# Kernel optimization log

Hardware: AMD Instinct MI355X
Metric: run time of the kernel (lower is better)

The kernel has to match this reference:

```python
import jax, jax.numpy as jnp
import numpy as np

B, CF, CC, H, W = 4, 64, 128, 512, 512
NUM_POINTS = 4096
OVERSAMPLE = 3
BETA = 0.75
HIDDEN = 256
OUT_CH = 4
IN_FEATS = CF + CC


def grid_sample_points(img, coords):
    """Bilinear sample img [B,C,H,W] at coords [B,N,2] in [0,1] (x,y order),
    matching F.grid_sample(align_corners=False, padding_mode='zeros') after
    the 2*coords-1 normalization in point_sample."""
    Bb, C, Hh, Ww = img.shape
    # unnormalize: ((2c-1)+1)*size/2 - 0.5 == c*size - 0.5
    x = coords[..., 0] * Ww - 0.5
    y = coords[..., 1] * Hh - 0.5
    x0 = jnp.floor(x)
    y0 = jnp.floor(y)
    wx1 = x - x0  # [B,N]
    wy1 = y - y0
    x0i = x0.astype(jnp.int32)
    y0i = y0.astype(jnp.int32)
    flat = img.reshape(Bb, C, Hh * Ww)

    def gather(xi, yi):
        valid = (xi >= 0) & (xi < Ww) & (yi >= 0) & (yi < Hh)
        idx = jnp.clip(yi, 0, Hh - 1) * Ww + jnp.clip(xi, 0, Ww - 1)
        v = jnp.take_along_axis(flat, idx[:, None, :], axis=2)  # [B,C,N]
        return v * valid[:, None, :].astype(img.dtype)

    out = (gather(x0i, y0i) * ((1.0 - wx1) * (1.0 - wy1))[:, None, :]
           + gather(x0i + 1, y0i) * (wx1 * (1.0 - wy1))[:, None, :]
           + gather(x0i, y0i + 1) * ((1.0 - wx1) * wy1)[:, None, :]
           + gather(x0i + 1, y0i + 1) * (wx1 * wy1)[:, None, :])
    return out  # [B,C,N]


def setup_inputs() -> dict:
    key = jax.random.key(0)
    ks = jax.random.split(key, 12)
    num_sampled = NUM_POINTS * OVERSAMPLE
    num_uncertain = int(BETA * NUM_POINTS)
    num_random = NUM_POINTS - num_uncertain
    s1 = 1.0 / np.sqrt(IN_FEATS)
    s2 = 1.0 / np.sqrt(HIDDEN)
    return {
        "fine_features": jax.random.normal(ks[0], (B, CF, H, W), jnp.float32),
        "coarse_features": jax.random.normal(ks[1], (B, CC, H, W), jnp.float32),
        "coarse_logits": jax.random.normal(ks[2], (B, OUT_CH, H, W), jnp.float32),
        "rand_points": jax.random.uniform(ks[3], (B, num_sampled, 2), jnp.float32),
        "rand_extra": jax.random.uniform(ks[4], (B, num_random, 2), jnp.float32),
        "W1": jax.random.uniform(ks[5], (HIDDEN, IN_FEATS), jnp.float32, -s1, s1),
        "b1": jax.random.uniform(ks[6], (HIDDEN,), jnp.float32, -s1, s1),
        "W2": jax.random.uniform(ks[7], (HIDDEN, HIDDEN), jnp.float32, -s2, s2),
        "b2": jax.random.uniform(ks[8], (HIDDEN,), jnp.float32, -s2, s2),
        "W3": jax.random.uniform(ks[9], (OUT_CH, HIDDEN), jnp.float32, -s2, s2),
        "b3": jax.random.uniform(ks[10], (OUT_CH,), jnp.float32, -s2, s2),
    }


def reference(fine_features, coarse_features, coarse_logits, rand_points,
              rand_extra, W1, b1, W2, b2, W3, b3):
    # 1) uncertainty at oversampled random points (channel 0 of coarse logits)
    pt_logits0 = grid_sample_points(coarse_logits, rand_points)[:, 0, :]  # [B,Ns]
    uncertainty = 1.0 - jnp.abs(jax.nn.sigmoid(pt_logits0) - 0.5) * 2.0
    num_uncertain = int(BETA * NUM_POINTS)
    _, idx = jax.lax.top_k(uncertainty, num_uncertain)  # [B,k]
    chosen_uncertain = jnp.take_along_axis(rand_points, idx[..., None], axis=1)
    points = jnp.concatenate([chosen_uncertain, rand_extra], axis=1)  # [B,N,2]
    # 2) gather fine + coarse features at selected points
    fine_s = grid_sample_points(fine_features, points)      # [B,Cf,N]
    coarse_s = grid_sample_points(coarse_features, points)  # [B,Cc,N]
    feats = jnp.concatenate([fine_s, coarse_s], axis=1).transpose(0, 2, 1)  # [B,N,Cin]
    # 3) pointwise MLP (torch Linear: x @ W.T + b)
    h = jax.nn.relu(feats @ W1.T + b1)
    h = jax.nn.relu(h @ W2.T + b2)
    point_logits = (h @ W3.T + b3).transpose(0, 2, 1)  # [B,out_ch,N]
    return point_logits, points
```

## Files before the change

kernel.cpp:

```cpp
#include <hip/hip_runtime.h>
#include <math.h>

#define BATCH 4
#define HW 512
#define NPLANE (512 * 512)
#define NS 12288
#define NU 3072
#define NR 1024
#define NP 4096
#define CF_CH 64
#define CC_CH 128
#define CIN 192
#define HID 256
#define OUTC 4
#define M_TOT (BATCH * NP)
#define GCH_SPLIT 4

__device__ __forceinline__ float xla_expf(float xin) {
  float x = fminf(fmaxf(xin, -88.3762626647949f), 88.3762626647950f);
  float fx = floorf(__fadd_rn(__fmul_rn(x, 1.44269504088896341f), 0.5f));
  float tmp = __fmul_rn(0.693359375f, fx);
  float z = __fmul_rn(-2.12194440e-4f, fx);
  x = __fsub_rn(__fsub_rn(x, tmp), z);
  float y = __fadd_rn(__fmul_rn(x, 1.9875691500E-4f), 1.3981999507E-3f);
  y = __fadd_rn(__fmul_rn(y, x), 8.3334519073E-3f);
  y = __fadd_rn(__fmul_rn(y, x), 4.1665795894E-2f);
  y = __fadd_rn(__fmul_rn(y, x), 1.6666665459E-1f);
  y = __fadd_rn(__fmul_rn(y, x), 5.0000001201E-1f);
  z = __fmul_rn(x, x);
  y = __fadd_rn(__fmul_rn(y, z), x);
  y = __fadd_rn(y, 1.0f);
  int n = (int)fx;
  float p2n = __int_as_float((n + 127) << 23);
  return __fmul_rn(y, p2n);
}

__global__ void k_uncert(const float* __restrict__ logits,
                         const float* __restrict__ rp,
                         float* __restrict__ u) {
  int gid = blockIdx.x * 256 + threadIdx.x;
  if (gid >= BATCH * NS) return;
  int b = gid / NS;
  float px = rp[(size_t)gid * 2 + 0];
  float py = rp[(size_t)gid * 2 + 1];
  const float* plane = logits + (size_t)b * OUTC * NPLANE;

  float x = __fsub_rn(__fmul_rn(px, 512.0f), 0.5f);
  float y = __fsub_rn(__fmul_rn(py, 512.0f), 0.5f);
  float x0f = floorf(x), y0f = floorf(y);
  float wx = __fsub_rn(x, x0f);
  float wy = __fsub_rn(y, y0f);
  int x0 = (int)x0f, y0 = (int)y0f;
  int x1 = x0 + 1, y1 = y0 + 1;
  bool vx0 = (x0 >= 0) & (x0 < HW);
  bool vx1 = (x1 >= 0) & (x1 < HW);
  bool vy0 = (y0 >= 0) & (y0 < HW);
  bool vy1 = (y1 >= 0) & (y1 < HW);
  float g00 = (vx0 && vy0) ? plane[y0 * HW + x0] : 0.0f;
  float g10 = (vx1 && vy0) ? plane[y0 * HW + x1] : 0.0f;
  float g01 = (vx0 && vy1) ? plane[y1 * HW + x0] : 0.0f;
  float g11 = (vx1 && vy1) ? plane[y1 * HW + x1] : 0.0f;
  float omx = __fsub_rn(1.0f, wx);
  float omy = __fsub_rn(1.0f, wy);
  float w00 = __fmul_rn(omx, omy);
  float w10 = __fmul_rn(wx, omy);
  float w01 = __fmul_rn(omx, wy);
  float w11 = __fmul_rn(wx, wy);
  float s = __fadd_rn(
      __fadd_rn(__fadd_rn(__fmul_rn(g00, w00), __fmul_rn(g10, w10)),
                __fmul_rn(g01, w01)),
      __fmul_rn(g11, w11));
  float e = xla_expf(-s);
  float sig = __fdiv_rn(1.0f, __fadd_rn(1.0f, e));
  float t = __fmul_rn(fabsf(__fsub_rn(sig, 0.5f)), 2.0f);
  u[gid] = __fsub_rn(1.0f, t);
}

__global__ __launch_bounds__(256) void k_select(const float* __restrict__ u,
                                                const float* __restrict__ rp,
                                                float* __restrict__ pts_out) {
  __shared__ __align__(16) float su[NS];
  int b = blockIdx.x / (NS / 256);
  int blk = blockIdx.x % (NS / 256);
  const float* ub = u + (size_t)b * NS;
  for (int t = threadIdx.x; t < NS / 4; t += 256)
    ((float4*)su)[t] = ((const float4*)ub)[t];
  __syncthreads();
  int i = blk * 256 + (int)threadIdx.x;
  int wb = i & ~63;
  float ui = su[i];
  int r0 = 0, r1 = 0, r2 = 0, r3 = 0;
  for (int j = 0; j < wb; j += 8) {
    float4 v = *(const float4*)&su[j];
    float4 w = *(const float4*)&su[j + 4];
    r0 += (v.x >= ui) + (w.x >= ui);
    r1 += (v.y >= ui) + (w.y >= ui);
    r2 += (v.z >= ui) + (w.z >= ui);
    r3 += (v.w >= ui) + (w.w >= ui);
  }
  for (int j = wb; j < wb + 64; ++j) {
    float vj = su[j];
    r0 += (vj > ui) || (vj == ui && j < i);
  }
  for (int j = wb + 64; j < NS; j += 8) {
    float4 v = *(const float4*)&su[j];
    float4 w = *(const float4*)&su[j + 4];
    r0 += (v.x > ui) + (w.x > ui);
    r1 += (v.y > ui) + (w.y > ui);
    r2 += (v.z > ui) + (w.z > ui);
    r3 += (v.w > ui) + (w.w > ui);
  }
  int rank = (r0 + r1) + (r2 + r3);
  if (rank < NU) {
    pts_out[((size_t)b * NP + rank) * 2 + 0] = rp[((size_t)b * NS + i) * 2 + 0];
    pts_out[((size_t)b * NP + rank) * 2 + 1] = rp[((size_t)b * NS + i) * 2 + 1];
  }
}

__global__ void k_extra(const float* __restrict__ re, float* __restrict__ pts_out) {
  int gid = blockIdx.x * 256 + threadIdx.x;
  if (gid >= BATCH * NR) return;
  int b = gid / NR, j = gid % NR;
  pts_out[((size_t)b * NP + NU + j) * 2 + 0] = re[(size_t)gid * 2 + 0];
  pts_out[((size_t)b * NP + NU + j) * 2 + 1] = re[(size_t)gid * 2 + 1];
}

__global__ void k_prep(const float* __restrict__ pts, int2* __restrict__ m2,
                       float4* __restrict__ wts) {
  int g = blockIdx.x * 256 + threadIdx.x;
  if (g >= M_TOT) return;
  float px = pts[(size_t)g * 2 + 0];
  float py = pts[(size_t)g * 2 + 1];
  float x = px * 512.0f - 0.5f;
  float y = py * 512.0f - 0.5f;
  float x0f = floorf(x), y0f = floorf(y);
  float wx = x - x0f, wy = y - y0f;
  int x0 = (int)x0f, y0 = (int)y0f;
  bool vx0 = (unsigned)x0 < (unsigned)HW;
  bool vx1 = (unsigned)(x0 + 1) < (unsigned)HW;
  bool vy0 = (unsigned)y0 < (unsigned)HW;
  bool vy1 = (unsigned)(y0 + 1) < (unsigned)HW;
  int vm = (int)(vx0 && vy0) | ((int)(vx1 && vy0) << 1) |
           ((int)(vx0 && vy1) << 2) | ((int)(vx1 && vy1) << 3);
  m2[g] = make_int2(y0 * HW + x0, vm);
  wts[g] = make_float4((1.0f - wx) * (1.0f - wy), wx * (1.0f - wy),
                       (1.0f - wx) * wy, wx * wy);
}

__global__ __launch_bounds__(256) void k_gather3(
    const float* __restrict__ fine, const float* __restrict__ coarse,
    const int2* __restrict__ m2, const float4* __restrict__ wts,
    float* __restrict__ featsT) {
  int c = blockIdx.x % CIN;
  int rem = blockIdx.x / CIN;
  int b = rem & (BATCH - 1);
  int part = rem >> 2;
  const float* plane = (c < CF_CH)
                           ? fine + ((size_t)b * CF_CH + c) * NPLANE
                           : coarse + ((size_t)b * CC_CH + (c - CF_CH)) * NPLANE;
  const int2* m2b = m2 + (size_t)b * NP;
  const float4* wtsb = wts + (size_t)b * NP;
  float* outrow = featsT + (size_t)c * M_TOT + (size_t)b * NP;
  int s0 = part * (NP / GCH_SPLIT);
#pragma unroll
  for (int q = 0; q < NP / GCH_SPLIT / 256; ++q) {
    int s = s0 + q * 256 + (int)threadIdx.x;
    int2 mm = m2b[s];
    float4 w = wtsb[s];
    const float* bp = plane + mm.x;
    float t00 = 0.0f, t10 = 0.0f, t01 = 0.0f, t11 = 0.0f;
    if (mm.y & 1) t00 = bp[0] * w.x;
    if (mm.y & 2) t10 = bp[1] * w.y;
    if (mm.y & 4) t01 = bp[HW] * w.z;
    if (mm.y & 8) t11 = bp[HW + 1] * w.w;
    outrow[s] = ((t00 + t10) + t01) + t11;
  }
}

__global__ __launch_bounds__(256) void k_gemm1_At(const float* __restrict__ At,
                                                  const float* __restrict__ W,
                                                  const float* __restrict__ bias,
                                                  float* __restrict__ C) {
  __shared__ __align__(16) float As[32][68];
  __shared__ __align__(16) float Bs[32][68];
  const int bx = blockIdx.x & 3;
  const int by = blockIdx.x >> 2;
  const int tid = threadIdx.x;
  const int tn = tid & 15, tm = tid >> 4;
  const int m_base = by * 64, n_base = bx * 64;
  float acc[4][4] = {};
  for (int k0 = 0; k0 < CIN; k0 += 32) {
#pragma unroll
    for (int r = 0; r < 2; ++r) {
      int t = tid + r * 256;
      int kk = t >> 4, mg = (t & 15) * 4;
      *(float4*)&As[kk][mg] =
          *(const float4*)&At[(size_t)(k0 + kk) * M_TOT + m_base + mg];
      int row = t >> 3, cg = (t & 7) * 4;
      float4 vw = *(const float4*)&W[(size_t)(n_base + row) * CIN + k0 + cg];
      Bs[cg + 0][row] = vw.x;
      Bs[cg + 1][row] = vw.y;
      Bs[cg + 2][row] = vw.z;
      Bs[cg + 3][row] = vw.w;
    }
    __syncthreads();
#pragma unroll
    for (int kk = 0; kk < 32; ++kk) {
      float4 a4 = *(const float4*)&As[kk][tm * 4];
      float4 b4 = *(const float4*)&Bs[kk][tn * 4];
      float av[4] = {a4.x, a4.y, a4.z, a4.w};
      float bw[4] = {b4.x, b4.y, b4.z, b4.w};
#pragma unroll
      for (int i = 0; i < 4; ++i)
#pragma unroll
        for (int j = 0; j < 4; ++j) acc[i][j] = fmaf(av[i], bw[j], acc[i][j]);
    }
    __syncthreads();
  }
  float bs[4];
#pragma unroll
  for (int j = 0; j < 4; ++j) bs[j] = bias[n_base + tn * 4 + j];
#pragma unroll
  for (int i = 0; i < 4; ++i) {
    float4 o;
    o.x = fmaxf(acc[i][0] + bs[0], 0.0f);
    o.y = fmaxf(acc[i][1] + bs[1], 0.0f);
    o.z = fmaxf(acc[i][2] + bs[2], 0.0f);
    o.w = fmaxf(acc[i][3] + bs[3], 0.0f);
    *(float4*)&C[(size_t)(m_base + tm * 4 + i) * HID + n_base + tn * 4] = o;
  }
}

template <int K>
__global__ __launch_bounds__(256) void k_gemm_relu(const float* __restrict__ A,
                                                   const float* __restrict__ W,
                                                   const float* __restrict__ bias,
                                                   float* __restrict__ C) {
  __shared__ __align__(16) float As[32][68];
  __shared__ __align__(16) float Bs[32][68];
  const int bx = blockIdx.x & 3;
  const int by = blockIdx.x >> 2;
  const int tid = threadIdx.x;
  const int tn = tid & 15, tm = tid >> 4;
  const int m_base = by * 64, n_base = bx * 64;
  float acc[4][4] = {};
  for (int k0 = 0; k0 < K; k0 += 32) {
#pragma unroll
    for (int r = 0; r < 2; ++r) {
      int t = tid + r * 256;
      int row = t >> 3, cg = (t & 7) * 4;
      float4 va = *(const float4*)&A[(size_t)(m_base + row) * K + k0 + cg];
      As[cg + 0][row] = va.x;
      As[cg + 1][row] = va.y;
      As[cg + 2][row] = va.z;
      As[cg + 3][row] = va.w;
      float4 vw = *(const float4*)&W[(size_t)(n_base + row) * K + k0 + cg];
      Bs[cg + 0][row] = vw.x;
      Bs[cg + 1][row] = vw.y;
      Bs[cg + 2][row] = vw.z;
      Bs[cg + 3][row] = vw.w;
    }
    __syncthreads();
#pragma unroll
    for (int kk = 0; kk < 32; ++kk) {
      float4 a4 = *(const float4*)&As[kk][tm * 4];
      float4 b4 = *(const float4*)&Bs[kk][tn * 4];
      float av[4] = {a4.x, a4.y, a4.z, a4.w};
      float bw[4] = {b4.x, b4.y, b4.z, b4.w};
#pragma unroll
      for (int i = 0; i < 4; ++i)
#pragma unroll
        for (int j = 0; j < 4; ++j) acc[i][j] = fmaf(av[i], bw[j], acc[i][j]);
    }
    __syncthreads();
  }
  float bs[4];
#pragma unroll
  for (int j = 0; j < 4; ++j) bs[j] = bias[n_base + tn * 4 + j];
#pragma unroll
  for (int i = 0; i < 4; ++i) {
    float4 o;
    o.x = fmaxf(acc[i][0] + bs[0], 0.0f);
    o.y = fmaxf(acc[i][1] + bs[1], 0.0f);
    o.z = fmaxf(acc[i][2] + bs[2], 0.0f);
    o.w = fmaxf(acc[i][3] + bs[3], 0.0f);
    *(float4*)&C[(size_t)(m_base + tm * 4 + i) * HID + n_base + tn * 4] = o;
  }
}

__global__ __launch_bounds__(256) void k_out(const float* __restrict__ h,
                                             const float* __restrict__ W3,
                                             const float* __restrict__ b3,
                                             float* __restrict__ out) {
  int gp = blockIdx.x * 4 + (threadIdx.x >> 6);
  int lane = threadIdx.x & 63;
  const float* hr = h + (size_t)gp * HID;
  float4 hv = *(const float4*)&hr[lane * 4];
  float s[4];
#pragma unroll
  for (int o = 0; o < 4; ++o) {
    float4 w = *(const float4*)&W3[o * HID + lane * 4];
    s[o] = hv.x * w.x + hv.y * w.y + hv.z * w.z + hv.w * w.w;
  }
#pragma unroll
  for (int off = 32; off; off >>= 1)
#pragma unroll
    for (int o = 0; o < 4; ++o) s[o] += __shfl_xor(s[o], off, 64);
  if (lane == 0) {
    int b = gp / NP, n = gp % NP;
#pragma unroll
    for (int o = 0; o < 4; ++o)
      out[((size_t)b * OUTC + o) * NP + n] = s[o] + b3[o];
  }
}

extern "C" void kernel_launch(void* const* d_in, const int* in_sizes, int n_in,
                              void* d_out, int out_size, void* d_ws, size_t ws_size,
                              hipStream_t stream) {
  const float* fine = (const float*)d_in[0];
  const float* coarse = (const float*)d_in[1];
  const float* logits = (const float*)d_in[2];
  const float* rand_points = (const float*)d_in[3];
  const float* rand_extra = (const float*)d_in[4];
  const float* W1 = (const float*)d_in[5];
  const float* b1 = (const float*)d_in[6];
  const float* W2 = (const float*)d_in[7];
  const float* b2 = (const float*)d_in[8];
  const float* W3 = (const float*)d_in[9];
  const float* b3 = (const float*)d_in[10];
  float* out = (float*)d_out;

  float* out_logits = out;
  float* out_points = out + (size_t)BATCH * OUTC * NP;

  char* ws = (char*)d_ws;
  float* u = (float*)(ws + 0);
  int2* m2 = (int2*)(ws + 196608);
  float4* wts = (float4*)(ws + 327680);
  float* featsT = (float*)(ws + 589824);
  float* h1 = (float*)(ws + 13172736);
  float* h2 = (float*)(ws + 29949952);

  k_uncert<<<(BATCH * NS + 255) / 256, 256, 0, stream>>>(logits, rand_points, u);
  k_select<<<BATCH * (NS / 256), 256, 0, stream>>>(u, rand_points, out_points);
  k_extra<<<(BATCH * NR + 255) / 256, 256, 0, stream>>>(rand_extra, out_points);
  k_prep<<<(M_TOT + 255) / 256, 256, 0, stream>>>(out_points, m2, wts);
  k_gather3<<<CIN * BATCH * GCH_SPLIT, 256, 0, stream>>>(fine, coarse, m2, wts,
                                                         featsT);
  k_gemm1_At<<<(M_TOT / 64) * 4, 256, 0, stream>>>(featsT, W1, b1, h1);
  k_gemm_relu<HID><<<(M_TOT / 64) * 4, 256, 0, stream>>>(h1, W2, b2, h2);
  k_out<<<M_TOT / 4, 256, 0, stream>>>(h2, W3, b3, out_logits);
}
```

Baseline: 326.4 us.

## Fuse extra-point copy into uncertainty kernel, inline prep into gather, drop LDS in select

Merges the rand_extra copy kernel into the uncertainty kernel and folds the point-prep computation (indices, validity mask, bilinear weights) into the gather kernel, removing two launches and the m2/wts intermediate buffers. The top-k rank kernel now reads uncertainties directly from global memory (through cache) instead of staging them in shared memory, and its comparison loops process 16 elements per iteration. The trade-off is that gather blocks recompute coordinates per channel, and select now depends on the cache hierarchy instead of LDS for its repeated scans.

```diff
diff --git a/kernel.cpp b/kernel.cpp
--- a/kernel.cpp
+++ b/kernel.cpp
@@ -35,80 +35,90 @@
   return __fmul_rn(y, p2n);
 }
 
-__global__ void k_uncert(const float* __restrict__ logits,
-                         const float* __restrict__ rp,
-                         float* __restrict__ u) {
+__global__ void k_uncert_extra(const float* __restrict__ logits,
+                               const float* __restrict__ rp,
+                               const float* __restrict__ re,
+                               float* __restrict__ u,
+                               float* __restrict__ pts_out) {
   int gid = blockIdx.x * 256 + threadIdx.x;
-  if (gid >= BATCH * NS) return;
-  int b = gid / NS;
-  float px = rp[(size_t)gid * 2 + 0];
-  float py = rp[(size_t)gid * 2 + 1];
-  const float* plane = logits + (size_t)b * OUTC * NPLANE;
-
-  float x = __fsub_rn(__fmul_rn(px, 512.0f), 0.5f);
-  float y = __fsub_rn(__fmul_rn(py, 512.0f), 0.5f);
-  float x0f = floorf(x), y0f = floorf(y);
-  float wx = __fsub_rn(x, x0f);
-  float wy = __fsub_rn(y, y0f);
-  int x0 = (int)x0f, y0 = (int)y0f;
-  int x1 = x0 + 1, y1 = y0 + 1;
-  bool vx0 = (x0 >= 0) & (x0 < HW);
-  bool vx1 = (x1 >= 0) & (x1 < HW);
-  bool vy0 = (y0 >= 0) & (y0 < HW);
-  bool vy1 = (y1 >= 0) & (y1 < HW);
-  float g00 = (vx0 && vy0) ? plane[y0 * HW + x0] : 0.0f;
-  float g10 = (vx1 && vy0) ? plane[y0 * HW + x1] : 0.0f;
-  float g01 = (vx0 && vy1) ? plane[y1 * HW + x0] : 0.0f;
-  float g11 = (vx1 && vy1) ? plane[y1 * HW + x1] : 0.0f;
-  float omx = __fsub_rn(1.0f, wx);
-  float omy = __fsub_rn(1.0f, wy);
-  float w00 = __fmul_rn(omx, omy);
-  float w10 = __fmul_rn(wx, omy);
-  float w01 = __fmul_rn(omx, wy);
-  float w11 = __fmul_rn(wx, wy);
-  float s = __fadd_rn(
-      __fadd_rn(__fadd_rn(__fmul_rn(g00, w00), __fmul_rn(g10, w10)),
-                __fmul_rn(g01, w01)),
-      __fmul_rn(g11, w11));
-  float e = xla_expf(-s);
-  float sig = __fdiv_rn(1.0f, __fadd_rn(1.0f, e));
-  float t = __fmul_rn(fabsf(__fsub_rn(sig, 0.5f)), 2.0f);
-  u[gid] = __fsub_rn(1.0f, t);
+  if (gid < BATCH * NS) {
+    int b = gid / NS;
+    float px = rp[(size_t)gid * 2 + 0];
+    float py = rp[(size_t)gid * 2 + 1];
+    const float* plane = logits + (size_t)b * OUTC * NPLANE;
+
+    float x = __fsub_rn(__fmul_rn(px, 512.0f), 0.5f);
+    float y = __fsub_rn(__fmul_rn(py, 512.0f), 0.5f);
+    float x0f = floorf(x), y0f = floorf(y);
+    float wx = __fsub_rn(x, x0f);
+    float wy = __fsub_rn(y, y0f);
+    int x0 = (int)x0f, y0 = (int)y0f;
+    int x1 = x0 + 1, y1 = y0 + 1;
+    bool vx0 = (x0 >= 0) & (x0 < HW);
+    bool vx1 = (x1 >= 0) & (x1 < HW);
+    bool vy0 = (y0 >= 0) & (y0 < HW);
+    bool vy1 = (y1 >= 0) & (y1 < HW);
+    float g00 = (vx0 && vy0) ? plane[y0 * HW + x0] : 0.0f;
+    float g10 = (vx1 && vy0) ? plane[y0 * HW + x1] : 0.0f;
+    float g01 = (vx0 && vy1) ? plane[y1 * HW + x0] : 0.0f;
+    float g11 = (vx1 && vy1) ? plane[y1 * HW + x1] : 0.0f;
+    float omx = __fsub_rn(1.0f, wx);
+    float omy = __fsub_rn(1.0f, wy);
+    float w00 = __fmul_rn(omx, omy);
+    float w10 = __fmul_rn(wx, omy);
+    float w01 = __fmul_rn(omx, wy);
+    float w11 = __fmul_rn(wx, wy);
+    float s = __fadd_rn(
+        __fadd_rn(__fadd_rn(__fmul_rn(g00, w00), __fmul_rn(g10, w10)),
+                  __fmul_rn(g01, w01)),
+        __fmul_rn(g11, w11));
+    float e = xla_expf(-s);
+    float sig = __fdiv_rn(1.0f, __fadd_rn(1.0f, e));
+    float t = __fmul_rn(fabsf(__fsub_rn(sig, 0.5f)), 2.0f);
+    u[gid] = __fsub_rn(1.0f, t);
+  } else {
+    int g = gid - BATCH * NS;
+    if (g < BATCH * NR) {
+      int b = g / NR, j = g - b * NR;
+      pts_out[((size_t)b * NP + NU + j) * 2 + 0] = re[(size_t)g * 2 + 0];
+      pts_out[((size_t)b * NP + NU + j) * 2 + 1] = re[(size_t)g * 2 + 1];
+    }
+  }
 }
 
 __global__ __launch_bounds__(256) void k_select(const float* __restrict__ u,
                                                 const float* __restrict__ rp,
                                                 float* __restrict__ pts_out) {
-  __shared__ __align__(16) float su[NS];
   int b = blockIdx.x / (NS / 256);
   int blk = blockIdx.x % (NS / 256);
-  const float* ub = u + (size_t)b * NS;
-  for (int t = threadIdx.x; t < NS / 4; t += 256)
-    ((float4*)su)[t] = ((const float4*)ub)[t];
-  __syncthreads();
+  const float* __restrict__ ub = u + (size_t)b * NS;
   int i = blk * 256 + (int)threadIdx.x;
   int wb = i & ~63;
-  float ui = su[i];
+  float ui = ub[i];
   int r0 = 0, r1 = 0, r2 = 0, r3 = 0;
-  for (int j = 0; j < wb; j += 8) {
-    float4 v = *(const float4*)&su[j];
-    float4 w = *(const float4*)&su[j + 4];
-    r0 += (v.x >= ui) + (w.x >= ui);
-    r1 += (v.y >= ui) + (w.y >= ui);
-    r2 += (v.z >= ui) + (w.z >= ui);
-    r3 += (v.w >= ui) + (w.w >= ui);
+  for (int j = 0; j < wb; j += 16) {
+    float4 v0 = *(const float4*)&ub[j];
+    float4 v1 = *(const float4*)&ub[j + 4];
+    float4 v2 = *(const float4*)&ub[j + 8];
+    float4 v3 = *(const float4*)&ub[j + 12];
+    r0 += (v0.x >= ui) + (v1.x >= ui) + (v2.x >= ui) + (v3.x >= ui);
+    r1 += (v0.y >= ui) + (v1.y >= ui) + (v2.y >= ui) + (v3.y >= ui);
+    r2 += (v0.z >= ui) + (v1.z >= ui) + (v2.z >= ui) + (v3.z >= ui);
+    r3 += (v0.w >= ui) + (v1.w >= ui) + (v2.w >= ui) + (v3.w >= ui);
   }
   for (int j = wb; j < wb + 64; ++j) {
-    float vj = su[j];
+    float vj = ub[j];
     r0 += (vj > ui) || (vj == ui && j < i);
   }
-  for (int j = wb + 64; j < NS; j += 8) {
-    float4 v = *(const float4*)&su[j];
-    float4 w = *(const float4*)&su[j + 4];
-    r0 += (v.x > ui) + (w.x > ui);
-    r1 += (v.y > ui) + (w.y > ui);
-    r2 += (v.z > ui) + (w.z > ui);
-    r3 += (v.w > ui) + (w.w > ui);
+  for (int j = wb + 64; j < NS; j += 16) {
+    float4 v0 = *(const float4*)&ub[j];
+    float4 v1 = *(const float4*)&ub[j + 4];
+    float4 v2 = *(const float4*)&ub[j + 8];
+    float4 v3 = *(const float4*)&ub[j + 12];
+    r0 += (v0.x > ui) + (v1.x > ui) + (v2.x > ui) + (v3.x > ui);
+    r1 += (v0.y > ui) + (v1.y > ui) + (v2.y > ui) + (v3.y > ui);
+    r2 += (v0.z > ui) + (v1.z > ui) + (v2.z > ui) + (v3.z > ui);
+    r3 += (v0.w > ui) + (v1.w > ui) + (v2.w > ui) + (v3.w > ui);
   }
   int rank = (r0 + r1) + (r2 + r3);
   if (rank < NU) {
@@ -117,40 +127,9 @@
   }
 }
 
-__global__ void k_extra(const float* __restrict__ re, float* __restrict__ pts_out) {
-  int gid = blockIdx.x * 256 + threadIdx.x;
-  if (gid >= BATCH * NR) return;
-  int b = gid / NR, j = gid % NR;
-  pts_out[((size_t)b * NP + NU + j) * 2 + 0] = re[(size_t)gid * 2 + 0];
-  pts_out[((size_t)b * NP + NU + j) * 2 + 1] = re[(size_t)gid * 2 + 1];
-}
-
-__global__ void k_prep(const float* __restrict__ pts, int2* __restrict__ m2,
-                       float4* __restrict__ wts) {
-  int g = blockIdx.x * 256 + threadIdx.x;
-  if (g >= M_TOT) return;
-  float px = pts[(size_t)g * 2 + 0];
-  float py = pts[(size_t)g * 2 + 1];
-  float x = px * 512.0f - 0.5f;
-  float y = py * 512.0f - 0.5f;
-  float x0f = floorf(x), y0f = floorf(y);
-  float wx = x - x0f, wy = y - y0f;
-  int x0 = (int)x0f, y0 = (int)y0f;
-  bool vx0 = (unsigned)x0 < (unsigned)HW;
-  bool vx1 = (unsigned)(x0 + 1) < (unsigned)HW;
-  bool vy0 = (unsigned)y0 < (unsigned)HW;
-  bool vy1 = (unsigned)(y0 + 1) < (unsigned)HW;
-  int vm = (int)(vx0 && vy0) | ((int)(vx1 && vy0) << 1) |
-           ((int)(vx0 && vy1) << 2) | ((int)(vx1 && vy1) << 3);
-  m2[g] = make_int2(y0 * HW + x0, vm);
-  wts[g] = make_float4((1.0f - wx) * (1.0f - wy), wx * (1.0f - wy),
-                       (1.0f - wx) * wy, wx * wy);
-}
-
-__global__ __launch_bounds__(256) void k_gather3(
+__global__ __launch_bounds__(256) void k_gather4(
     const float* __restrict__ fine, const float* __restrict__ coarse,
-    const int2* __restrict__ m2, const float4* __restrict__ wts,
-    float* __restrict__ featsT) {
+    const float* __restrict__ pts, float* __restrict__ featsT) {
   int c = blockIdx.x % CIN;
   int rem = blockIdx.x / CIN;
   int b = rem & (BATCH - 1);
@@ -158,21 +137,29 @@
   const float* plane = (c < CF_CH)
                            ? fine + ((size_t)b * CF_CH + c) * NPLANE
                            : coarse + ((size_t)b * CC_CH + (c - CF_CH)) * NPLANE;
-  const int2* m2b = m2 + (size_t)b * NP;
-  const float4* wtsb = wts + (size_t)b * NP;
+  const float* pb = pts + (size_t)b * NP * 2;
   float* outrow = featsT + (size_t)c * M_TOT + (size_t)b * NP;
   int s0 = part * (NP / GCH_SPLIT);
 #pragma unroll
   for (int q = 0; q < NP / GCH_SPLIT / 256; ++q) {
     int s = s0 + q * 256 + (int)threadIdx.x;
-    int2 mm = m2b[s];
-    float4 w = wtsb[s];
-    const float* bp = plane + mm.x;
+    float px = pb[2 * s + 0];
+    float py = pb[2 * s + 1];
+    float x = px * 512.0f - 0.5f;
+    float y = py * 512.0f - 0.5f;
+    float x0f = floorf(x), y0f = floorf(y);
+    float wx = x - x0f, wy = y - y0f;
+    int x0 = (int)x0f, y0 = (int)y0f;
+    bool vx0 = (unsigned)x0 < (unsigned)HW;
+    bool vx1 = (unsigned)(x0 + 1) < (unsigned)HW;
+    bool vy0 = (unsigned)y0 < (unsigned)HW;
+    bool vy1 = (unsigned)(y0 + 1) < (unsigned)HW;
+    const float* bp = plane + (y0 * HW + x0);
     float t00 = 0.0f, t10 = 0.0f, t01 = 0.0f, t11 = 0.0f;
-    if (mm.y & 1) t00 = bp[0] * w.x;
-    if (mm.y & 2) t10 = bp[1] * w.y;
-    if (mm.y & 4) t01 = bp[HW] * w.z;
-    if (mm.y & 8) t11 = bp[HW + 1] * w.w;
+    if (vx0 && vy0) t00 = bp[0] * ((1.0f - wx) * (1.0f - wy));
+    if (vx1 && vy0) t10 = bp[1] * (wx * (1.0f - wy));
+    if (vx0 && vy1) t01 = bp[HW] * ((1.0f - wx) * wy);
+    if (vx1 && vy1) t11 = bp[HW + 1] * (wx * wy);
     outrow[s] = ((t00 + t10) + t01) + t11;
   }
 }
@@ -335,18 +322,15 @@
 
   char* ws = (char*)d_ws;
   float* u = (float*)(ws + 0);
-  int2* m2 = (int2*)(ws + 196608);
-  float4* wts = (float4*)(ws + 327680);
-  float* featsT = (float*)(ws + 589824);
-  float* h1 = (float*)(ws + 13172736);
-  float* h2 = (float*)(ws + 29949952);
-
-  k_uncert<<<(BATCH * NS + 255) / 256, 256, 0, stream>>>(logits, rand_points, u);
+  float* featsT = (float*)(ws + 196608);
+  float* h1 = (float*)(ws + 12779520);
+  float* h2 = (float*)(ws + 29556736);
+
+  k_uncert_extra<<<(BATCH * NS + BATCH * NR + 255) / 256, 256, 0, stream>>>(
+      logits, rand_points, rand_extra, u, out_points);
   k_select<<<BATCH * (NS / 256), 256, 0, stream>>>(u, rand_points, out_points);
-  k_extra<<<(BATCH * NR + 255) / 256, 256, 0, stream>>>(rand_extra, out_points);
-  k_prep<<<(M_TOT + 255) / 256, 256, 0, stream>>>(out_points, m2, wts);
-  k_gather3<<<CIN * BATCH * GCH_SPLIT, 256, 0, stream>>>(fine, coarse, m2, wts,
-                                                         featsT);
+  k_gather4<<<CIN * BATCH * GCH_SPLIT, 256, 0, stream>>>(fine, coarse,
+                                                         out_points, featsT);
   k_gemm1_At<<<(M_TOT / 64) * 4, 256, 0, stream>>>(featsT, W1, b1, h1);
   k_gemm_relu<HID><<<(M_TOT / 64) * 4, 256, 0, stream>>>(h1, W2, b2, h2);
   k_out<<<M_TOT / 4, 256, 0, stream>>>(h2, W3, b3, out_logits);
```

New measurement: 404.9 us. 1.24x slower.

## Bucket-sort sample points by image row to localize bilinear gathers

Applied to the files above, without the earlier changes.

Adds a per-batch counting sort of the selected points by image row (the top-left pixel index shifted right by 9). The point indices and weights are permuted into sorted order before the feature gather, and the output scatter uses the permutation to restore the original point order. The aim is better cache and TLB locality for the random-access bilinear gather over the 512x512 feature planes, at the cost of two extra small kernels and an indirect write in the final output stage. The MLP stages run in sorted order, which is fine because they work on each point independently.

```diff
diff --git a/kernel.cpp b/kernel.cpp
--- a/kernel.cpp
+++ b/kernel.cpp
@@ -147,9 +147,52 @@
                        (1.0f - wx) * wy, wx * wy);
 }
 
-__global__ __launch_bounds__(256) void k_gather3(
+__global__ __launch_bounds__(512) void k_sort(const int2* __restrict__ m2,
+                                              int* __restrict__ perm) {
+  __shared__ int hist[512], pref[512];
+  int b = blockIdx.x, tid = threadIdx.x;
+  hist[tid] = 0;
+  __syncthreads();
+  for (int p = tid; p < NP; p += 512) {
+    int i00 = m2[(size_t)b * NP + p].x;
+    int key = min(max(i00, 0), NPLANE - 1) >> 9;
+    atomicAdd(&hist[key], 1);
+  }
+  __syncthreads();
+  int v = hist[tid];
+  pref[tid] = v;
+  __syncthreads();
+  for (int d = 1; d < 512; d <<= 1) {
+    int t = (tid >= d) ? pref[tid - d] : 0;
+    __syncthreads();
+    pref[tid] += t;
+    __syncthreads();
+  }
+  hist[tid] = pref[tid] - v;
+  __syncthreads();
+  for (int p = tid; p < NP; p += 512) {
+    int i00 = m2[(size_t)b * NP + p].x;
+    int key = min(max(i00, 0), NPLANE - 1) >> 9;
+    int pos = atomicAdd(&hist[key], 1);
+    perm[(size_t)b * NP + pos] = p;
+  }
+}
+
+__global__ void k_reorder(const int* __restrict__ perm,
+                          const int2* __restrict__ m2,
+                          const float4* __restrict__ wts,
+                          int2* __restrict__ m2s, float4* __restrict__ wtss) {
+  int gid = blockIdx.x * 256 + threadIdx.x;
+  if (gid >= M_TOT) return;
+  int b = gid / NP;
+  int p = perm[gid];
+  m2s[gid] = m2[(size_t)b * NP + p];
+  wtss[gid] = wts[(size_t)b * NP + p];
+}
+
+__global__ __launch_bounds__(256) void k_gather5(
     const float* __restrict__ fine, const float* __restrict__ coarse,
-    const int2* __restrict__ m2, const float4* __restrict__ wts,
+    const int2* __restrict__ m2s, const float4* __restrict__ wtss,
     float* __restrict__ featsT) {
   int c = blockIdx.x % CIN;
   int rem = blockIdx.x / CIN;
@@ -158,8 +201,8 @@
   const float* plane = (c < CF_CH)
                            ? fine + ((size_t)b * CF_CH + c) * NPLANE
                            : coarse + ((size_t)b * CC_CH + (c - CF_CH)) * NPLANE;
-  const int2* m2b = m2 + (size_t)b * NP;
-  const float4* wtsb = wts + (size_t)b * NP;
+  const int2* m2b = m2s + (size_t)b * NP;
+  const float4* wtsb = wtss + (size_t)b * NP;
   float* outrow = featsT + (size_t)c * M_TOT + (size_t)b * NP;
   int s0 = part * (NP / GCH_SPLIT);
 #pragma unroll
@@ -291,6 +334,7 @@
 __global__ __launch_bounds__(256) void k_out(const float* __restrict__ h,
                                              const float* __restrict__ W3,
                                              const float* __restrict__ b3,
+                                             const int* __restrict__ perm,
                                              float* __restrict__ out) {
   int gp = blockIdx.x * 4 + (threadIdx.x >> 6);
   int lane = threadIdx.x & 63;
@@ -307,7 +351,8 @@
 #pragma unroll
     for (int o = 0; o < 4; ++o) s[o] += __shfl_xor(s[o], off, 64);
   if (lane == 0) {
-    int b = gp / NP, n = gp % NP;
+    int b = gp / NP, ns = gp % NP;
+    int n = perm[(size_t)b * NP + ns];
 #pragma unroll
     for (int o = 0; o < 4; ++o)
       out[((size_t)b * OUTC + o) * NP + n] = s[o] + b3[o];
@@ -337,17 +382,22 @@
   float* u = (float*)(ws + 0);
   int2* m2 = (int2*)(ws + 196608);
   float4* wts = (float4*)(ws + 327680);
-  float* featsT = (float*)(ws + 589824);
-  float* h1 = (float*)(ws + 13172736);
-  float* h2 = (float*)(ws + 29949952);
+  int2* m2s = (int2*)(ws + 589824);
+  float4* wtss = (float4*)(ws + 720896);
+  int* perm = (int*)(ws + 983040);
+  float* featsT = (float*)(ws + 1048576);
+  float* h1 = (float*)(ws + 13631488);
+  float* h2 = (float*)(ws + 30408704);
 
   k_uncert<<<(BATCH * NS + 255) / 256, 256, 0, stream>>>(logits, rand_points, u);
   k_select<<<BATCH * (NS / 256), 256, 0, stream>>>(u, rand_points, out_points);
   k_extra<<<(BATCH * NR + 255) / 256, 256, 0, stream>>>(rand_extra, out_points);
   k_prep<<<(M_TOT + 255) / 256, 256, 0, stream>>>(out_points, m2, wts);
-  k_gather3<<<CIN * BATCH * GCH_SPLIT, 256, 0, stream>>>(fine, coarse, m2, wts,
-                                                         featsT);
+  k_sort<<<BATCH, 512, 0, stream>>>(m2, perm);
+  k_reorder<<<(M_TOT + 255) / 256, 256, 0, stream>>>(perm, m2, wts, m2s, wtss);
+  k_gather5<<<CIN * BATCH * GCH_SPLIT, 256, 0, stream>>>(fine, coarse, m2s,
+                                                         wtss, featsT);
   k_gemm1_At<<<(M_TOT / 64) * 4, 256, 0, stream>>>(featsT, W1, b1, h1);
   k_gemm_relu<HID><<<(M_TOT / 64) * 4, 256, 0, stream>>>(h1, W2, b2, h2);
-  k_out<<<M_TOT / 4, 256, 0, stream>>>(h2, W3, b3, out_logits);
-}
+  k_out<<<M_TOT / 4, 256, 0, stream>>>(h2, W3, b3, perm, out_logits);
+}
```

Result: faster. 306.0 us (-6.3%).
